# Kernel optimization log

Hardware: AMD Instinct MI355X
Metric: run time of the kernel (lower is better)

The kernel has to match this reference:

```python
import jax, jax.numpy as jnp
import numpy as np

BATCH = 2048
N_MOL = 16
HEADS = 8      # C
A_DIM = 64     # embedding_dim
B_DIM = 64     # output_dim
D_IN = 64
POS_DIM = 6
CA = HEADS * A_DIM
CB = HEADS * B_DIM


def _pos_encoding(n_mol):
    # get_pos_encoding_(pos, C=6, dim_embedding=3): 3 sin + 3 cos terms
    def enc(p):
        return np.array([np.sin(p / 6.0 ** (2 * i / 3.0)) for i in (1, 2, 3)]
                        + [np.cos(p / 6.0 ** (2 * i / 3.0)) for i in (1, 2, 3)])
    return np.stack([enc(i) for i in range(n_mol)]).astype(np.float32)  # (n_mol, 6)


def setup_inputs() -> dict:
    key = jax.random.key(0)
    ks = jax.random.split(key, 8)
    d_ext = D_IN + POS_DIM

    def w(k, fi, fo):
        return jax.random.normal(k, (fi, fo), jnp.float32) / np.sqrt(fi).astype(np.float32)

    return {
        "x": jax.random.normal(ks[0], (BATCH, N_MOL, D_IN), jnp.float32),
        "flow_mask": jnp.ones((N_MOL,), jnp.float32),
        "Wk_h": w(ks[1], d_ext, CA), "bk_h": jnp.zeros((CA,), jnp.float32),
        "Wk_o": w(ks[2], CA, CA),    "bk_o": jnp.zeros((CA,), jnp.float32),
        "Wq_h": w(ks[3], d_ext, CA), "bq_h": jnp.zeros((CA,), jnp.float32),
        "Wq_o": w(ks[4], CA, CA),    "bq_o": jnp.zeros((CA,), jnp.float32),
        "Wv_h": w(ks[5], d_ext, CB), "bv_h": jnp.zeros((CB,), jnp.float32),
        "Wv_o": w(ks[6], CB, CB),    "bv_o": jnp.zeros((CB,), jnp.float32),
        "pos_emb": jnp.asarray(_pos_encoding(N_MOL)),
    }


def reference(x, flow_mask, Wk_h, bk_h, Wk_o, bk_o, Wq_h, bq_h, Wq_o, bq_o,
              Wv_h, bv_h, Wv_o, bv_o, pos_emb):
    batch = x.shape[0]
    # one_hot_extend_: append positional encoding per molecule -> (b, n_mol, d_in+6)
    xe = jnp.concatenate(
        [x, jnp.broadcast_to(pos_emb[None], (batch, N_MOL, POS_DIM))], axis=-1)

    def mlp(Wh, bh, Wo, bo):  # 1 silu hidden layer + linear output
        return jax.nn.silu(xe @ Wh + bh) @ Wo + bo

    k = mlp(Wk_h, bk_h, Wk_o, bk_o).reshape(batch, N_MOL, HEADS, A_DIM)
    q = mlp(Wq_h, bq_h, Wq_o, bq_o).reshape(batch, N_MOL, HEADS, A_DIM)
    v = mlp(Wv_h, bv_h, Wv_o, bv_o).reshape(batch, N_MOL, HEADS, B_DIM)

    norm = 1.0 / np.sqrt(A_DIM).astype(np.float32)
    # scores over molecule pairs, per head: (b, i, j, c)
    arg = jnp.einsum('i,j,bica,bjca->bijc', flow_mask, flow_mask, k, q) * norm
    w = jax.nn.softplus(arg) + 1e-5
    mask_self = 1.0 - jnp.eye(N_MOL, dtype=x.dtype)  # mask_self=True, n_mol>1
    w = w * mask_self[None, :, :, None]
    w = w / jnp.sum(w, axis=-2, keepdims=True)  # normalize over j
    # weighted combine, summing over j and heads c -> (b, n_mol, B)
    return jnp.einsum('j,bijc,bjcd->bid', flow_mask, w, v)
```

## Files before the change

### kernel.cpp

```cpp
#include <hip/hip_runtime.h>
#include <hip/hip_bf16.h>

typedef __hip_bfloat16 bf16;
typedef __attribute__((ext_vector_type(8))) short bf16x8;
typedef __attribute__((ext_vector_type(4))) float floatx4;
typedef unsigned short ushort;
typedef unsigned int uint;

#define ROWS 32768
#define KX 96

#define MFMA(a, b, c) __builtin_amdgcn_mfma_f32_16x16x32_bf16(a, b, c, 0, 0, 0)

__device__ __forceinline__ ushort f2bf(float f) {
  union { float f; unsigned int i; } u; u.f = f;
  return (ushort)((u.i + 0x7fffu + ((u.i >> 16) & 1u)) >> 16);
}

__global__ void prep_misc(const float* __restrict__ x, const float* __restrict__ pos,
    const float* __restrict__ bk1, const float* __restrict__ bq1, const float* __restrict__ bv1,
    const float* __restrict__ bk2, const float* __restrict__ bq2, const float* __restrict__ bv2,
    bf16* __restrict__ xe, float* __restrict__ b1, float* __restrict__ b2)
{
  int idx = blockIdx.x * 256 + threadIdx.x;
  if (idx < ROWS * KX) {
    int r = idx / KX, col = idx - r * KX;
    float v = 0.f;
    if (col < 64)      v = x[r * 64 + col];
    else if (col < 70) v = pos[(r & 15) * 6 + (col - 64)];
    xe[idx] = __float2bfloat16(v);
  } else if (idx < ROWS * KX + 3072) {
    int i = idx - ROWS * KX;
    if (i < 1536) {
      int z = i >> 9, nl = i & 511;
      const float* s = (z == 0) ? bk1 : (z == 1) ? bq1 : bv1;
      b1[i] = s[nl];
    } else {
      int j = i - 1536;
      int z = j >> 9, nl = j & 511;
      const float* s = (z == 0) ? bk2 : (z == 1) ? bq2 : bv2;
      b2[j] = s[nl];
    }
  }
}

__global__ __launch_bounds__(256) void prep_wt(
    const float* __restrict__ Wk_h, const float* __restrict__ Wq_h, const float* __restrict__ Wv_h,
    const float* __restrict__ Wk_o, const float* __restrict__ Wq_o, const float* __restrict__ Wv_o,
    bf16* __restrict__ w1t, bf16* __restrict__ w2t)
{
  __shared__ float tile[32][33];
  const int bid = blockIdx.x;
  const int c = threadIdx.x & 31, r0 = threadIdx.x >> 5;
  if (bid < 768) {
    const int z = bid >> 8, rem = bid & 255;
    const int nt = rem >> 4, kt = rem & 15;
    const float* src = (z == 0) ? Wk_o : (z == 1) ? Wq_o : Wv_o;
    #pragma unroll
    for (int rr = 0; rr < 4; ++rr) {
      int r = r0 + rr * 8;
      tile[r][c] = src[(kt * 32 + r) * 512 + nt * 32 + c];
    }
    __syncthreads();
    #pragma unroll
    for (int rr = 0; rr < 4; ++rr) {
      int r = r0 + rr * 8;
      w2t[((long)z * 512 + nt * 32 + r) * 512 + kt * 32 + c] = __float2bfloat16(tile[c][r]);
    }
  } else {
    const int b2i = bid - 768;
    const int z = b2i / 48, rem = b2i - z * 48;
    const int kt = rem >> 4, nt = rem & 15;
    const float* src = (z == 0) ? Wk_h : (z == 1) ? Wq_h : Wv_h;
    #pragma unroll
    for (int rr = 0; rr < 4; ++rr) {
      int r = r0 + rr * 8;
      int k = kt * 32 + r;
      tile[r][c] = (k < 70) ? src[k * 512 + nt * 32 + c] : 0.f;
    }
    __syncthreads();
    #pragma unroll
    for (int rr = 0; rr < 4; ++rr) {
      int r = r0 + rr * 8;
      w1t[((long)z * 512 + nt * 32 + r) * KX + kt * 32 + c] = __float2bfloat16(tile[c][r]);
    }
  }
}

template<int SILU, int G2>
__global__ __launch_bounds__(256) void mlp_gemm(
    const bf16* __restrict__ A, int lda,
    const bf16* __restrict__ Bt, int ldb,
    const float* __restrict__ bias,
    bf16* __restrict__ C, int ldc, int K)
{
  __shared__ __align__(16) bf16 As[128 * 32];
  __shared__ __align__(16) bf16 Bs[128 * 32];
  const int tid  = threadIdx.x;
  const int wave = tid >> 6, lane = tid & 63;

  const int bid = blockIdx.x;
  const int xcd = bid & 7;
  const int l   = bid >> 3;
  const int ml  = l / 12;
  const int nn  = l - ml * 12;
  const int bm  = (xcd * 32 + ml) * 128;
  const int bnf = nn * 128;
  const int z   = bnf >> 9;

  const bf16* Ap = A + (G2 ? z * 512 : 0);
  const int wm = (wave >> 1) * 64;
  const int wn = (wave & 1) * 64;

  floatx4 acc[4][4] = {};
  const int arow = lane >> 2;
  const int acol = (lane & 3) * 8;

  for (int k0 = 0; k0 < K; k0 += 32) {
    __syncthreads();
    #pragma unroll
    for (int ch = 0; ch < 2; ++ch) {
      const int rb = wave * 32 + ch * 16;
      const bf16* ga = Ap + (long)(bm + rb + arow) * lda + k0 + acol;
      const bf16* gb = Bt + (long)(bnf + rb + arow) * ldb + k0 + acol;
      __builtin_amdgcn_global_load_lds(
          (const __attribute__((address_space(1))) unsigned int*)ga,
          (__attribute__((address_space(3))) unsigned int*)(As + rb * 32), 16, 0, 0);
      __builtin_amdgcn_global_load_lds(
          (const __attribute__((address_space(1))) unsigned int*)gb,
          (__attribute__((address_space(3))) unsigned int*)(Bs + rb * 32), 16, 0, 0);
    }
    asm volatile("s_waitcnt vmcnt(0)" ::: "memory");
    __syncthreads();

    bf16x8 af[4], bfr[4];
    #pragma unroll
    for (int mi = 0; mi < 4; ++mi)
      af[mi] = *(const bf16x8*)(As + (wm + mi * 16 + (lane & 15)) * 32 + (lane >> 4) * 8);
    #pragma unroll
    for (int ni = 0; ni < 4; ++ni)
      bfr[ni] = *(const bf16x8*)(Bs + (wn + ni * 16 + (lane & 15)) * 32 + (lane >> 4) * 8);
    #pragma unroll
    for (int mi = 0; mi < 4; ++mi)
      #pragma unroll
      for (int ni = 0; ni < 4; ++ni)
        acc[mi][ni] = MFMA(af[mi], bfr[ni], acc[mi][ni]);
  }

  if (!G2 || z < 2) {
    bf16* Cz = G2 ? (C + (long)z * ROWS * 512) : C;
    #pragma unroll
    for (int mi = 0; mi < 4; ++mi) {
      #pragma unroll
      for (int ni = 0; ni < 4; ++ni) {
        const int ncf = bnf + wn + ni * 16 + (lane & 15);
        const int nc  = G2 ? (ncf & 511) : ncf;
        const float bv = bias[ncf];
        #pragma unroll
        for (int r = 0; r < 4; ++r) {
          const long m = bm + wm + mi * 16 + (lane >> 4) * 4 + r;
          float v = acc[mi][ni][r] + bv;
          if (SILU) v = v / (1.f + __expf(-v));
          Cz[m * (long)ldc + nc] = __float2bfloat16(v);
        }
      }
    }
  } else {
    ushort* vt = (ushort*)C + (long)2 * ROWS * 512;
    #pragma unroll
    for (int mi = 0; mi < 4; ++mi) {
      const int m0 = bm + wm + mi * 16;
      const long bb = (long)(m0 >> 4) * 8192;
      #pragma unroll
      for (int ni = 0; ni < 4; ++ni) {
        const int ncf = bnf + wn + ni * 16 + (lane & 15);
        const int nc  = ncf & 511;
        const float bv = bias[ncf];
        float v0 = acc[mi][ni][0] + bv, v1 = acc[mi][ni][1] + bv;
        float v2 = acc[mi][ni][2] + bv, v3 = acc[mi][ni][3] + bv;
        uint2 pk;
        pk.x = (uint)f2bf(v0) | ((uint)f2bf(v1) << 16);
        pk.y = (uint)f2bf(v2) | ((uint)f2bf(v3) << 16);
        *(uint2*)(vt + bb + (long)nc * 16 + (lane >> 4) * 4) = pk;
      }
    }
  }
}

__global__ __launch_bounds__(256) void attn_v3(
    const bf16* __restrict__ kqv,
    const float* __restrict__ flow_mask,
    float* __restrict__ out)
{
  __shared__ ushort wn_s[4 * 16 * 40];
  __shared__ float  fm_s[16];

  const int tid  = threadIdx.x;
  const int lane = tid & 63;
  const int wave = tid >> 6;
  const int bid  = blockIdx.x;
  const int b    = (bid & 7) * 256 + (bid >> 3);

  if (tid < 16) fm_s[tid] = flow_mask[tid];
  __syncthreads();

  const int jcol = lane & 15;
  const int rgrp = lane >> 4;
  const int ko   = rgrp * 8;

  {
    const bf16* kg = kqv + ((long)b * 16 + jcol) * 512;
    const bf16* qg = kg + 16777216;
    const float fmj = fm_s[jcol];
    #pragma unroll
    for (int h = 0; h < 2; ++h) {
      const int c = wave + h * 4;
      floatx4 acc = {0.f, 0.f, 0.f, 0.f};
      bf16x8 a0 = *(const bf16x8*)(kg + c * 64 + ko);
      bf16x8 a1 = *(const bf16x8*)(kg + c * 64 + 32 + ko);
      bf16x8 b0 = *(const bf16x8*)(qg + c * 64 + ko);
      bf16x8 b1 = *(const bf16x8*)(qg + c * 64 + 32 + ko);
      acc = MFMA(a0, b0, acc);
      acc = MFMA(a1, b1, acc);

      float wv[4], ss[4];
      #pragma unroll
      for (int r = 0; r < 4; ++r) {
        const int i = rgrp * 4 + r;
        float arg = acc[r] * (fm_s[i] * fmj * 0.125f);
        float sp  = fmaxf(arg, 0.f) + log1pf(__expf(-fabsf(arg)));
        float wvv = sp + 1e-5f;
        if (i == jcol) wvv = 0.f;
        wv[r] = wvv; ss[r] = wvv;
      }
      #pragma unroll
      for (int m = 1; m < 16; m <<= 1) {
        #pragma unroll
        for (int r = 0; r < 4; ++r) ss[r] += __shfl_xor(ss[r], m);
      }
      const int hp = c >> 1, chl = c & 1;
      #pragma unroll
      for (int r = 0; r < 4; ++r) {
        const int i = rgrp * 4 + r;
        wn_s[hp * 640 + i * 40 + chl * 16 + jcol] = f2bf(wv[r] / ss[r] * fmj);
      }
    }
  }
  __syncthreads();

  {
    const int dcol = wave * 16 + jcol;
    const ushort* vb = (const ushort*)kqv + (long)2 * ROWS * 512 + (long)b * 8192;
    floatx4 o = {0.f, 0.f, 0.f, 0.f};
    #pragma unroll
    for (int hp = 0; hp < 4; ++hp) {
      bf16x8 af = *(const bf16x8*)&wn_s[hp * 640 + jcol * 40 + ko];
      const int c  = 2 * hp + (ko >> 4);
      const int jb = ko & 15;
      bf16x8 bfr = *(const bf16x8*)(vb + (long)(c * 64 + dcol) * 16 + jb);
      o = MFMA(af, bfr, o);
    }
    float* ob = out + (long)b * 1024 + dcol;
    #pragma unroll
    for (int r = 0; r < 4; ++r) ob[(rgrp * 4 + r) * 64] = o[r];
  }
}

extern "C" void kernel_launch(void* const* d_in, const int* in_sizes, int n_in,
                              void* d_out, int out_size, void* d_ws, size_t ws_size,
                              hipStream_t stream) {
  const float* x    = (const float*)d_in[0];
  const float* fmk  = (const float*)d_in[1];
  const float* Wk_h = (const float*)d_in[2];
  const float* bk_h = (const float*)d_in[3];
  const float* Wk_o = (const float*)d_in[4];
  const float* bk_o = (const float*)d_in[5];
  const float* Wq_h = (const float*)d_in[6];
  const float* bq_h = (const float*)d_in[7];
  const float* Wq_o = (const float*)d_in[8];
  const float* bq_o = (const float*)d_in[9];
  const float* Wv_h = (const float*)d_in[10];
  const float* bv_h = (const float*)d_in[11];
  const float* Wv_o = (const float*)d_in[12];
  const float* bv_o = (const float*)d_in[13];
  const float* pos  = (const float*)d_in[14];
  float* out = (float*)d_out;

  char* ws = (char*)d_ws;
  bf16*  xe  = (bf16*)(ws + 0);
  bf16*  w1t = (bf16*)(ws + 6291456);
  bf16*  w2t = (bf16*)(ws + 6586368);
  float* b1  = (float*)(ws + 8159232);
  float* b2  = (float*)(ws + 8165376);
  bf16*  hid = (bf16*)(ws + 8171520);
  bf16*  kqv = (bf16*)(ws + 108834816);
  if (ws_size < 209498112ULL) return;

  prep_misc<<<12300, 256, 0, stream>>>(x, pos, bk_h, bq_h, bv_h, bk_o, bq_o, bv_o,
                                       xe, b1, b2);
  prep_wt<<<912, 256, 0, stream>>>(Wk_h, Wq_h, Wv_h, Wk_o, Wq_o, Wv_o, w1t, w2t);
  mlp_gemm<1, 0><<<3072, 256, 0, stream>>>(xe, KX, w1t, KX, b1, hid, 1536, KX);
  mlp_gemm<0, 1><<<3072, 256, 0, stream>>>(hid, 1536, w2t, 512, b2, kqv, 512, 512);
  attn_v3<<<2048, 256, 0, stream>>>(kqv, fmk, out);
}
```

Measured before the change: 244.4 us.

## Split MLP GEMMs: register-resident first GEMM and double-buffered second GEMM

The shared templated GEMM is replaced by two specialized kernels. The first GEMM (K=96) keeps the whole A tile in registers and streams weight fragments directly from global memory without LDS, and writes paired bf16 outputs via a lane shuffle. The second GEMM double-buffers its LDS tiles so the next k-slice loads while MFMAs run on the current one. Both kernels use plain 2D grids instead of the XCD-aware block swizzle, and the attention kernel drops its swizzle too, which may hurt L2 locality.

New measurement: 262.4 us. 1.07x slower.

```diff
diff --git a/kernel.cpp b/kernel.cpp
--- a/kernel.cpp
+++ b/kernel.cpp
@@ -11,6 +11,9 @@
 #define KX 96
 
 #define MFMA(a, b, c) __builtin_amdgcn_mfma_f32_16x16x32_bf16(a, b, c, 0, 0, 0)
+#define GL_LDS(gp, lp) __builtin_amdgcn_global_load_lds( \
+    (const __attribute__((address_space(1))) unsigned int*)(gp), \
+    (__attribute__((address_space(3))) unsigned int*)(lp), 16, 0, 0)
 
 __device__ __forceinline__ ushort f2bf(float f) {
   union { float f; unsigned int i; } u; u.f = f;
@@ -87,81 +90,128 @@
   }
 }
 
-template<int SILU, int G2>
-__global__ __launch_bounds__(256) void mlp_gemm(
-    const bf16* __restrict__ A, int lda,
-    const bf16* __restrict__ Bt, int ldb,
+__global__ __launch_bounds__(256, 3) void gemm1_reg(
+    const bf16* __restrict__ xe, const bf16* __restrict__ w1t,
+    const float* __restrict__ bias, bf16* __restrict__ hid)
+{
+  const int tid = threadIdx.x, w = tid >> 6, lane = tid & 63;
+  const int r0 = blockIdx.x * 64;
+  const int bn = blockIdx.y * 256;
+  const int rowl = lane & 15, kg = (lane >> 4) * 8;
+
+  bf16x8 a0, a1, a2;
+  {
+    const bf16* xp = xe + (long)(r0 + 16 * w + rowl) * KX + kg;
+    a0 = *(const bf16x8*)xp;
+    a1 = *(const bf16x8*)(xp + 32);
+    a2 = *(const bf16x8*)(xp + 64);
+  }
+
+  floatx4 acc[16];
+  #pragma unroll
+  for (int nt = 0; nt < 16; ++nt) acc[nt] = (floatx4){0.f, 0.f, 0.f, 0.f};
+
+  const bf16* wp = w1t + (long)(bn + rowl) * KX + kg;
+  #pragma unroll
+  for (int nt = 0; nt < 16; ++nt) {
+    const bf16* bp = wp + (long)nt * 16 * KX;
+    bf16x8 b0 = *(const bf16x8*)bp;
+    bf16x8 b1 = *(const bf16x8*)(bp + 32);
+    bf16x8 b2 = *(const bf16x8*)(bp + 64);
+    acc[nt] = MFMA(a0, b0, acc[nt]);
+    acc[nt] = MFMA(a1, b1, acc[nt]);
+    acc[nt] = MFMA(a2, b2, acc[nt]);
+  }
+
+  const int m0 = r0 + 16 * w + (lane >> 4) * 4;
+  #pragma unroll
+  for (int nt = 0; nt < 16; ++nt) {
+    const int col = bn + nt * 16 + rowl;
+    const float bv = bias[col];
+    #pragma unroll
+    for (int r = 0; r < 4; ++r) {
+      float v = acc[nt][r] + bv;
+      v = v / (1.f + __expf(-v));
+      float vp = __shfl_xor(v, 1);
+      if (!(rowl & 1)) {
+        uint pk = (uint)f2bf(v) | ((uint)f2bf(vp) << 16);
+        *(uint*)(hid + (long)(m0 + r) * 1536 + col) = pk;
+      }
+    }
+  }
+}
+
+__global__ __launch_bounds__(256) void mlp_gemm2(
+    const bf16* __restrict__ A,
+    const bf16* __restrict__ Bt,
     const float* __restrict__ bias,
-    bf16* __restrict__ C, int ldc, int K)
-{
-  __shared__ __align__(16) bf16 As[128 * 32];
-  __shared__ __align__(16) bf16 Bs[128 * 32];
+    bf16* __restrict__ C)
+{
+  __shared__ __align__(16) bf16 As[2][128 * 32];
+  __shared__ __align__(16) bf16 Bs[2][128 * 32];
   const int tid  = threadIdx.x;
   const int wave = tid >> 6, lane = tid & 63;
-
-  const int bid = blockIdx.x;
-  const int xcd = bid & 7;
-  const int l   = bid >> 3;
-  const int ml  = l / 12;
-  const int nn  = l - ml * 12;
-  const int bm  = (xcd * 32 + ml) * 128;
-  const int bnf = nn * 128;
-  const int z   = bnf >> 9;
-
-  const bf16* Ap = A + (G2 ? z * 512 : 0);
+  const int z  = blockIdx.y >> 2;
+  const int bn = (blockIdx.y & 3) * 128;
+  const int bm = blockIdx.x * 128;
+  const int bnf = z * 512 + bn;
+  const bf16* Ap  = A + z * 512;
+  const bf16* Btp = Bt + (long)z * 512 * 512;
   const int wm = (wave >> 1) * 64;
   const int wn = (wave & 1) * 64;
-
-  floatx4 acc[4][4] = {};
   const int arow = lane >> 2;
   const int acol = (lane & 3) * 8;
 
-  for (int k0 = 0; k0 < K; k0 += 32) {
-    __syncthreads();
-    #pragma unroll
-    for (int ch = 0; ch < 2; ++ch) {
-      const int rb = wave * 32 + ch * 16;
-      const bf16* ga = Ap + (long)(bm + rb + arow) * lda + k0 + acol;
-      const bf16* gb = Bt + (long)(bnf + rb + arow) * ldb + k0 + acol;
-      __builtin_amdgcn_global_load_lds(
-          (const __attribute__((address_space(1))) unsigned int*)ga,
-          (__attribute__((address_space(3))) unsigned int*)(As + rb * 32), 16, 0, 0);
-      __builtin_amdgcn_global_load_lds(
-          (const __attribute__((address_space(1))) unsigned int*)gb,
-          (__attribute__((address_space(3))) unsigned int*)(Bs + rb * 32), 16, 0, 0);
-    }
-    asm volatile("s_waitcnt vmcnt(0)" ::: "memory");
-    __syncthreads();
-
+#define STAGE2(buf, t) do {                                                   \
+    const int k0_ = (t) * 32;                                                 \
+    _Pragma("unroll")                                                         \
+    for (int ch = 0; ch < 2; ++ch) {                                          \
+      const int rb = wave * 32 + ch * 16;                                     \
+      GL_LDS(Ap  + (long)(bm + rb + arow) * 1536 + k0_ + acol, As[buf] + rb * 32); \
+      GL_LDS(Btp + (long)(bn + rb + arow) * 512  + k0_ + acol, Bs[buf] + rb * 32); \
+    } } while (0)
+
+  STAGE2(0, 0);
+  asm volatile("s_waitcnt vmcnt(0)" ::: "memory");
+  __syncthreads();
+
+  floatx4 acc[4][4] = {};
+  int cur = 0;
+  for (int t = 0; t < 16; ++t) {
+    if (t + 1 < 16) STAGE2(cur ^ 1, t + 1);
     bf16x8 af[4], bfr[4];
     #pragma unroll
     for (int mi = 0; mi < 4; ++mi)
-      af[mi] = *(const bf16x8*)(As + (wm + mi * 16 + (lane & 15)) * 32 + (lane >> 4) * 8);
+      af[mi] = *(const bf16x8*)(As[cur] + (wm + mi * 16 + (lane & 15)) * 32 + (lane >> 4) * 8);
     #pragma unroll
     for (int ni = 0; ni < 4; ++ni)
-      bfr[ni] = *(const bf16x8*)(Bs + (wn + ni * 16 + (lane & 15)) * 32 + (lane >> 4) * 8);
+      bfr[ni] = *(const bf16x8*)(Bs[cur] + (wn + ni * 16 + (lane & 15)) * 32 + (lane >> 4) * 8);
     #pragma unroll
     for (int mi = 0; mi < 4; ++mi)
       #pragma unroll
       for (int ni = 0; ni < 4; ++ni)
         acc[mi][ni] = MFMA(af[mi], bfr[ni], acc[mi][ni]);
-  }
-
-  if (!G2 || z < 2) {
-    bf16* Cz = G2 ? (C + (long)z * ROWS * 512) : C;
+    if (t + 1 < 16) {
+      asm volatile("s_waitcnt vmcnt(0)" ::: "memory");
+      __syncthreads();
+      cur ^= 1;
+    }
+  }
+#undef STAGE2
+
+  if (z < 2) {
+    bf16* Cz = C + (long)z * ROWS * 512;
     #pragma unroll
     for (int mi = 0; mi < 4; ++mi) {
       #pragma unroll
       for (int ni = 0; ni < 4; ++ni) {
         const int ncf = bnf + wn + ni * 16 + (lane & 15);
-        const int nc  = G2 ? (ncf & 511) : ncf;
+        const int nc  = ncf & 511;
         const float bv = bias[ncf];
         #pragma unroll
         for (int r = 0; r < 4; ++r) {
           const long m = bm + wm + mi * 16 + (lane >> 4) * 4 + r;
-          float v = acc[mi][ni][r] + bv;
-          if (SILU) v = v / (1.f + __expf(-v));
-          Cz[m * (long)ldc + nc] = __float2bfloat16(v);
+          Cz[m * 512 + nc] = __float2bfloat16(acc[mi][ni][r] + bv);
         }
       }
     }
@@ -198,8 +248,7 @@
   const int tid  = threadIdx.x;
   const int lane = tid & 63;
   const int wave = tid >> 6;
-  const int bid  = blockIdx.x;
-  const int b    = (bid & 7) * 256 + (bid >> 3);
+  const int b    = blockIdx.x;
 
   if (tid < 16) fm_s[tid] = flow_mask[tid];
   __syncthreads();
@@ -299,7 +348,7 @@
   prep_misc<<<12300, 256, 0, stream>>>(x, pos, bk_h, bq_h, bv_h, bk_o, bq_o, bv_o,
                                        xe, b1, b2);
   prep_wt<<<912, 256, 0, stream>>>(Wk_h, Wq_h, Wv_h, Wk_o, Wq_o, Wv_o, w1t, w2t);
-  mlp_gemm<1, 0><<<3072, 256, 0, stream>>>(xe, KX, w1t, KX, b1, hid, 1536, KX);
-  mlp_gemm<0, 1><<<3072, 256, 0, stream>>>(hid, 1536, w2t, 512, b2, kqv, 512, 512);
+  gemm1_reg<<<dim3(512, 6), 256, 0, stream>>>(xe, w1t, b1, hid);
+  mlp_gemm2<<<dim3(256, 12), 256, 0, stream>>>(hid, w2t, b2, kqv);
   attn_v3<<<2048, 256, 0, stream>>>(kqv, fmk, out);
 }
```
